# Kernel tuning notes

Hardware: AMD Instinct MI355X
Metric: run time of the kernel (lower is better)

The kernel has to match this reference:

```python
import jax, jax.numpy as jnp
import numpy as np

DIM = 128
K = 16


def knn_points(xyz, new_xyz, k):
    # squared-distance matrix [B, M, N]
    dist = -2.0 * jnp.einsum('bmd,bnd->bmn', new_xyz, xyz)
    dist = dist + jnp.sum(new_xyz ** 2, -1, keepdims=True)
    dist = dist + jnp.sum(xyz ** 2, -1)[:, None, :]
    _, idx = jax.lax.top_k(-dist, k)  # smallest distances
    return idx  # [B, M, k]


def index_points(points, idx):
    # points [B, N, C], idx [B, M, k] -> [B, M, k, C]
    B, M, k = idx.shape
    C = points.shape[-1]
    flat = jnp.take_along_axis(points, idx.reshape(B, M * k, 1), axis=1)
    return flat.reshape(B, M, k, C)


def linear(x, w, b):
    return x @ w + b


def setup_inputs() -> dict:
    key = jax.random.key(0)
    ks = jax.random.split(key, 16)
    s = 0.02
    d = DIM
    inp = {
        'xyz': jax.random.normal(ks[0], (2, 8192, 3), jnp.float32),
        'features': jax.random.normal(ks[1], (2, 8192, d), jnp.float32),
        'wq': jax.random.normal(ks[2], (d, d), jnp.float32) * s,
        'bq': jnp.zeros((d,), jnp.float32),
        'wk': jax.random.normal(ks[3], (d, d), jnp.float32) * s,
        'bk': jnp.zeros((d,), jnp.float32),
        'wv': jax.random.normal(ks[4], (d, d), jnp.float32) * s,
        'bv': jnp.zeros((d,), jnp.float32),
        'pos_w1': jax.random.normal(ks[5], (3, d), jnp.float32) * s,
        'pos_b1': jnp.zeros((d,), jnp.float32),
        'pos_w2': jax.random.normal(ks[6], (d, d), jnp.float32) * s,
        'pos_b2': jnp.zeros((d,), jnp.float32),
        'attn_w1': jax.random.normal(ks[7], (d, d), jnp.float32) * s,
        'attn_b1': jnp.zeros((d,), jnp.float32),
        'attn_w2': jax.random.normal(ks[8], (d, d), jnp.float32) * s,
        'attn_b2': jnp.zeros((d,), jnp.float32),
    }
    return inp


def reference(xyz, features, wq, bq, wk, bk, wv, bv,
              pos_w1, pos_b1, pos_w2, pos_b2,
              attn_w1, attn_b1, attn_w2, attn_b2):
    idx = knn_points(xyz, xyz, K)  # [B, N, K]
    q = linear(features, wq, bq)
    k = linear(features, wk, bk)
    v = linear(features, wv, bv)
    k_g = index_points(k, idx)      # [B, N, K, C]
    v_g = index_points(v, idx)      # [B, N, K, C]
    xyz_g = index_points(xyz, idx)  # [B, N, K, 3]
    pos_diff = xyz[:, :, None, :] - xyz_g
    delta = linear(jax.nn.relu(linear(pos_diff, pos_w1, pos_b1)), pos_w2, pos_b2)
    attn_in = q[:, :, None, :] - k_g + delta
    attn = linear(jax.nn.relu(linear(attn_in, attn_w1, attn_b1)), attn_w2, attn_b2)
    attn = jax.nn.softmax(attn, axis=2)  # softmax over neighbor axis, per channel
    out = jnp.sum(attn * (v_g + delta), axis=2)  # [B, N, C]
    return out
```

## Files before the change

kernel.cpp:

```cpp
#include <hip/hip_runtime.h>
#include <math.h>

typedef unsigned short u16;
typedef unsigned int u32;
typedef __attribute__((ext_vector_type(8))) short short8b;
typedef __attribute__((ext_vector_type(4))) float f32x4;

#define N_PTS 8192
#define NTOT 16384
#define D 128
#define KNN 16
#define NCH_M 8
#define NCH_S 16
#define CAP 20

__device__ __forceinline__ u16 f2bf(float x) {
    u32 u = __float_as_uint(x);
    u = (u + 0x7FFFu + ((u >> 16) & 1u)) >> 16;
    return (u16)u;
}
__device__ __forceinline__ float bf2f(u16 v) {
    return __uint_as_float(((u32)v) << 16);
}

__global__ __launch_bounds__(256) void xyz4_prep(const float* __restrict__ xyz,
                                                 float4* __restrict__ xyz4) {
    const int i = blockIdx.x * 256 + threadIdx.x;
    const float x = xyz[i * 3 + 0], y = xyz[i * 3 + 1], z = xyz[i * 3 + 2];
    xyz4[i] = make_float4(x, y, z, 0.5f * (x * x + y * y + z * z));
}

__global__ __launch_bounds__(128) void knn_minslots(const float4* __restrict__ xyz4,
                                                    float* __restrict__ pmins) {
    __shared__ float4 tile[1024];
    const int tid = threadIdx.x;
    const int qA = blockIdx.x * 256 + tid;
    const int qB = qA + 128;
    const int cbase = (qA >> 13) * N_PTS + blockIdx.y * 1024;

    const float4 a = xyz4[qA];
    const float4 b = xyz4[qB];

    for (int i = tid; i < 1024; i += 128) tile[i] = xyz4[cbase + i];
    __syncthreads();

    float sA[16], sB[16];
#pragma unroll
    for (int s = 0; s < 16; ++s) { sA[s] = 1e30f; sB[s] = 1e30f; }

    for (int j0 = 0; j0 < 1024; j0 += 16) {
#pragma unroll
        for (int s = 0; s < 16; ++s) {
            const float4 c = tile[j0 + s];
            const float eA = fmaf(-a.x, c.x, fmaf(-a.y, c.y, fmaf(-a.z, c.z, c.w)));
            const float eB = fmaf(-b.x, c.x, fmaf(-b.y, c.y, fmaf(-b.z, c.z, c.w)));
            sA[s] = fminf(sA[s], eA);
            sB[s] = fminf(sB[s], eB);
        }
    }
#pragma unroll
    for (int s = 0; s < 16; ++s) {
        pmins[(size_t)(blockIdx.y * 16 + s) * NTOT + qA] = sA[s];
        pmins[(size_t)(blockIdx.y * 16 + s) * NTOT + qB] = sB[s];
    }
}

__global__ __launch_bounds__(256) void knn_thresh(const float* __restrict__ pmins,
                                                  float* __restrict__ thr) {
    const int g = blockIdx.x * 256 + threadIdx.x;
    float m[16];
#pragma unroll
    for (int s = 0; s < 16; ++s) m[s] = 1e30f;
    for (int ch = 0; ch < NCH_M; ++ch) {
#pragma unroll
        for (int s = 0; s < 16; ++s)
            m[s] = fminf(m[s], pmins[(size_t)(ch * 16 + s) * NTOT + g]);
    }
    float T = m[0];
#pragma unroll
    for (int s = 1; s < 16; ++s) T = fmaxf(T, m[s]);
    u32 u = __float_as_uint(T);
    u = (T >= 0.f) ? (u + 1u) : (u - 1u);
    thr[g] = __uint_as_float(u);
}

__global__ __launch_bounds__(256) void knn_select(const float4* __restrict__ xyz4,
                                                  const float* __restrict__ thr,
                                                  float* __restrict__ dcomp,
                                                  u16* __restrict__ jcomp) {
    __shared__ float4 tile[512];
    const int tid = threadIdx.x;
    const int ch = blockIdx.y;
    const int qA = blockIdx.x * 512 + tid;
    const int qB = qA + 256;
    const int cbase = (qA >> 13) * N_PTS + ch * 512;

    const float4 a = xyz4[qA];
    const float4 b = xyz4[qB];
    const float tA = thr[qA];
    const float tB = thr[qB];

    for (int i = tid; i < 512; i += 256) tile[i] = xyz4[cbase + i];
    __syncthreads();

    int cntA = 0, cntB = 0;
#pragma unroll 8
    for (int j = 0; j < 512; ++j) {
        const float4 c = tile[j];
        const float eA = fmaf(-a.x, c.x, fmaf(-a.y, c.y, fmaf(-a.z, c.z, c.w)));
        const float eB = fmaf(-b.x, c.x, fmaf(-b.y, c.y, fmaf(-b.z, c.z, c.w)));
        if (eA < tA) {
            if (cntA < CAP) {
                dcomp[(size_t)(ch * CAP + cntA) * NTOT + qA] = eA;
                jcomp[(size_t)(ch * CAP + cntA) * NTOT + qA] = (u16)j;
            }
            ++cntA;
        }
        if (eB < tB) {
            if (cntB < CAP) {
                dcomp[(size_t)(ch * CAP + cntB) * NTOT + qB] = eB;
                jcomp[(size_t)(ch * CAP + cntB) * NTOT + qB] = (u16)j;
            }
            ++cntB;
        }
    }
    for (int t = min(cntA, CAP); t < CAP; ++t)
        dcomp[(size_t)(ch * CAP + t) * NTOT + qA] = 1e30f;
    for (int t = min(cntB, CAP); t < CAP; ++t)
        dcomp[(size_t)(ch * CAP + t) * NTOT + qB] = 1e30f;
}

__global__ __launch_bounds__(64) void knn_merge(const float* __restrict__ dcomp,
                                                const u16* __restrict__ jcomp,
                                                int* __restrict__ knn_out) {
    const int g = blockIdx.x * 64 + threadIdx.x;
    const int bbase = (g >> 13) * N_PTS;
    float dist[KNN];
    int idx[KNN];
#pragma unroll
    for (int s = 0; s < KNN; ++s) { dist[s] = 1e30f; idx[s] = 0; }

    for (int ch = 0; ch < NCH_S; ++ch) {
        float d[CAP];
        int jj[CAP];
#pragma unroll
        for (int t = 0; t < CAP; ++t) {
            d[t] = dcomp[(size_t)(ch * CAP + t) * NTOT + g];
            jj[t] = (int)jcomp[(size_t)(ch * CAP + t) * NTOT + g];
        }
#pragma unroll
        for (int t = 0; t < CAP; ++t) {
            if (d[t] < dist[KNN - 1]) {
                dist[KNN - 1] = d[t];
                idx[KNN - 1] = bbase + ch * 512 + jj[t];
#pragma unroll
                for (int s = KNN - 1; s > 0; --s) {
                    if (dist[s] < dist[s - 1]) {
                        const float td = dist[s]; dist[s] = dist[s - 1]; dist[s - 1] = td;
                        const int ti = idx[s]; idx[s] = idx[s - 1]; idx[s - 1] = ti;
                    }
                }
            }
        }
    }
#pragma unroll
    for (int s = 0; s < KNN; ++s) knn_out[g * KNN + s] = idx[s];
}

__global__ __launch_bounds__(256) void qkv_kernel(const float* __restrict__ feat,
                                                  const float* __restrict__ wq, const float* __restrict__ bq,
                                                  const float* __restrict__ wk, const float* __restrict__ bk,
                                                  const float* __restrict__ wv, const float* __restrict__ bv,
                                                  float* __restrict__ qbuf, u16* __restrict__ kb,
                                                  u16* __restrict__ vb) {
    __shared__ float ftile[64][D];
    const int r0 = blockIdx.x * 64;

    const float* src = feat + (size_t)r0 * D;
    for (int i = threadIdx.x; i < 64 * D / 4; i += 256) {
        ((float4*)&ftile[0][0])[i] = ((const float4*)src)[i];
    }
    __syncthreads();

    const int col = threadIdx.x & (D - 1);
    const int rbase = (threadIdx.x >> 7) * 32;

    float accq[32], acck[32], accv[32];
    const float bqv = bq[col], bkv = bk[col], bvv = bv[col];
#pragma unroll
    for (int r = 0; r < 32; ++r) { accq[r] = bqv; acck[r] = bkv; accv[r] = bvv; }

    for (int i = 0; i < D; i += 4) {
        const float wq0 = wq[(i + 0) * D + col], wq1 = wq[(i + 1) * D + col];
        const float wq2 = wq[(i + 2) * D + col], wq3 = wq[(i + 3) * D + col];
        const float wk0 = wk[(i + 0) * D + col], wk1 = wk[(i + 1) * D + col];
        const float wk2 = wk[(i + 2) * D + col], wk3 = wk[(i + 3) * D + col];
        const float wv0 = wv[(i + 0) * D + col], wv1 = wv[(i + 1) * D + col];
        const float wv2 = wv[(i + 2) * D + col], wv3 = wv[(i + 3) * D + col];
#pragma unroll
        for (int r = 0; r < 32; ++r) {
            const float4 f = *(const float4*)&ftile[rbase + r][i];
            accq[r] = fmaf(f.x, wq0, accq[r]); accq[r] = fmaf(f.y, wq1, accq[r]);
            accq[r] = fmaf(f.z, wq2, accq[r]); accq[r] = fmaf(f.w, wq3, accq[r]);
            acck[r] = fmaf(f.x, wk0, acck[r]); acck[r] = fmaf(f.y, wk1, acck[r]);
            acck[r] = fmaf(f.z, wk2, acck[r]); acck[r] = fmaf(f.w, wk3, acck[r]);
            accv[r] = fmaf(f.x, wv0, accv[r]); accv[r] = fmaf(f.y, wv1, accv[r]);
            accv[r] = fmaf(f.z, wv2, accv[r]); accv[r] = fmaf(f.w, wv3, accv[r]);
        }
    }
#pragma unroll
    for (int r = 0; r < 32; ++r) {
        const size_t o = (size_t)(r0 + rbase + r) * D + col;
        qbuf[o] = accq[r]; kb[o] = f2bf(acck[r]); vb[o] = f2bf(accv[r]);
    }
}

__global__ __launch_bounds__(256) void pack_w(const float* __restrict__ pw2,
                                              const float* __restrict__ aw1,
                                              const float* __restrict__ aw2,
                                              u16* __restrict__ wp) {
    const int i = blockIdx.x * 256 + threadIdx.x;
    const int m = i >> 14;
    const int r = i & 16383;
    const int j = r & 7, l = (r >> 3) & 63, t = (r >> 9) & 7, q = r >> 12;
    const float* w = (m == 0) ? pw2 : (m == 1) ? aw1 : aw2;
    wp[i] = f2bf(w[(q * 32 + 8 * (l >> 4) + j) * D + t * 16 + (l & 15)]);
}

__device__ __forceinline__ void gemm_tile(const char* atile, const u16* wl, int mat,
                                          const float* brow, int a, int c2, int lane,
                                          f32x4 acc[2][2]) {
    const int c16 = lane & 15, grp = lane >> 4;
#pragma unroll
    for (int mt = 0; mt < 2; ++mt)
#pragma unroll
        for (int ct = 0; ct < 2; ++ct) {
            const float b = brow[c2 * 32 + ct * 16 + c16];
            acc[mt][ct] = (f32x4){b, b, b, b};
        }
#pragma unroll
    for (int q = 0; q < 4; ++q) {
        short8b af[2], bf[2];
#pragma unroll
        for (int mt = 0; mt < 2; ++mt) {
            const int row = (2 * a + mt) * 16 + c16;
            const int byte = (row * 256 + (q * 32 + grp * 8) * 2) ^ ((row & 7) << 4);
            af[mt] = *(const short8b*)(atile + byte);
        }
#pragma unroll
        for (int ct = 0; ct < 2; ++ct) {
            const int tg = c2 * 2 + ct;
            bf[ct] = *(const short8b*)((const char*)wl + (size_t)mat * 32768 +
                                       (size_t)((q * 8 + tg) * 64 + lane) * 16);
        }
#pragma unroll
        for (int mt = 0; mt < 2; ++mt)
#pragma unroll
            for (int ct = 0; ct < 2; ++ct)
                acc[mt][ct] = __builtin_amdgcn_mfma_f32_16x16x32_bf16(af[mt], bf[ct], acc[mt][ct], 0, 0, 0);
    }
}

__global__ __launch_bounds__(1024, 4) void fused_v3(const float* __restrict__ xyz,
                                                    const float* __restrict__ qbuf,
                                                    const u16* __restrict__ kb,
                                                    const u16* __restrict__ vb,
                                                    const int* __restrict__ knn_in,
                                                    const u16* __restrict__ wpack,
                                                    const float* __restrict__ pw1,
                                                    const float* __restrict__ pb1,
                                                    const float* __restrict__ pb2,
                                                    const float* __restrict__ ab1,
                                                    const float* __restrict__ ab2,
                                                    float* __restrict__ out) {
    __shared__ __align__(16) u16 wlds[49152];
    __shared__ __align__(16) char atile[32768];
    __shared__ float pw1s[3][D];
    __shared__ float pb1s[D];
    __shared__ float bias[3][D];
    __shared__ float diffs[128][4];
    __shared__ int nbrs[128];

    const int tid = threadIdx.x;
    {
        const uint4* s = (const uint4*)wpack;
        uint4* d = (uint4*)wlds;
        for (int i = tid; i < 6144; i += 1024) d[i] = s[i];
        if (tid < 384) pw1s[tid >> 7][tid & 127] = pw1[tid];
        if (tid < 128) pb1s[tid] = pb1[tid];
        else if (tid < 256) bias[0][tid & 127] = pb2[tid & 127];
        else if (tid < 512 && tid >= 384) bias[1][tid & 127] = ab1[tid & 127];
        else if (tid >= 512 && tid < 640) bias[2][tid & 127] = ab2[tid & 127];
    }

    const int wid = tid >> 6, lane = tid & 63;
    const int a = wid >> 2, c2 = wid & 3;
    const int c16 = lane & 15, grp = lane >> 4;

    for (int g = 0; g < 8; ++g) {
        const int p0 = blockIdx.x * 64 + g * 8;
        __syncthreads();

        if (tid < 128) {
            const int pt = p0 + (tid >> 4);
            const int nb = knn_in[pt * KNN + (tid & 15)];
            nbrs[tid] = nb;
            diffs[tid][0] = xyz[pt * 3 + 0] - xyz[nb * 3 + 0];
            diffs[tid][1] = xyz[pt * 3 + 1] - xyz[nb * 3 + 1];
            diffs[tid][2] = xyz[pt * 3 + 2] - xyz[nb * 3 + 2];
        }
        __syncthreads();

        {
            const int row = tid >> 3;
            const int c0 = (tid & 7) * 16;
            const float d0 = diffs[row][0], d1 = diffs[row][1], d2 = diffs[row][2];
#pragma unroll
            for (int c = 0; c < 16; c += 2) {
                const int cc = c0 + c;
                float h0 = pb1s[cc];
                h0 = fmaf(d0, pw1s[0][cc], h0); h0 = fmaf(d1, pw1s[1][cc], h0); h0 = fmaf(d2, pw1s[2][cc], h0);
                float h1 = pb1s[cc + 1];
                h1 = fmaf(d0, pw1s[0][cc + 1], h1); h1 = fmaf(d1, pw1s[1][cc + 1], h1); h1 = fmaf(d2, pw1s[2][cc + 1], h1);
                const u32 packed = (u32)f2bf(fmaxf(h0, 0.f)) | ((u32)f2bf(fmaxf(h1, 0.f)) << 16);
                const int byte = (row * 256 + cc * 2) ^ ((row & 7) << 4);
                *(u32*)(atile + byte) = packed;
            }
        }
        __syncthreads();

        f32x4 del[2][2];
        gemm_tile(atile, wlds, 0, bias[0], a, c2, lane, del);
        __syncthreads();

#pragma unroll
        for (int mt = 0; mt < 2; ++mt) {
            const int pt = p0 + 2 * a + mt;
#pragma unroll
            for (int ct = 0; ct < 2; ++ct) {
                const int col = c2 * 32 + ct * 16 + c16;
                const float qv = qbuf[(size_t)pt * D + col];
#pragma unroll
                for (int r = 0; r < 4; ++r) {
                    const int lrow = (2 * a + mt) * 16 + grp * 4 + r;
                    const int nb = nbrs[lrow];
                    const float kg = bf2f(kb[(size_t)nb * D + col]);
                    const float v = qv - kg + del[mt][ct][r];
                    const int byte = (lrow * 256 + col * 2) ^ ((lrow & 7) << 4);
                    *(u16*)(atile + byte) = f2bf(v);
                }
            }
        }
        __syncthreads();

        f32x4 acc[2][2];
        gemm_tile(atile, wlds, 1, bias[1], a, c2, lane, acc);
        __syncthreads();

#pragma unroll
        for (int mt = 0; mt < 2; ++mt)
#pragma unroll
            for (int ct = 0; ct < 2; ++ct) {
                const int col = c2 * 32 + ct * 16 + c16;
#pragma unroll
                for (int r = 0; r < 4; ++r) {
                    const int lrow = (2 * a + mt) * 16 + grp * 4 + r;
                    const int byte = (lrow * 256 + col * 2) ^ ((lrow & 7) << 4);
                    *(u16*)(atile + byte) = f2bf(fmaxf(acc[mt][ct][r], 0.f));
                }
            }
        __syncthreads();

        gemm_tile(atile, wlds, 2, bias[2], a, c2, lane, acc);

        float om[2][2];
#pragma unroll
        for (int mt = 0; mt < 2; ++mt) {
#pragma unroll
            for (int ct = 0; ct < 2; ++ct) {
                const int col = c2 * 32 + ct * 16 + c16;
                float vg[4];
#pragma unroll
                for (int r = 0; r < 4; ++r) {
                    const int lrow = (2 * a + mt) * 16 + grp * 4 + r;
                    vg[r] = bf2f(vb[(size_t)nbrs[lrow] * D + col]);
                }
                float m = fmaxf(fmaxf(acc[mt][ct][0], acc[mt][ct][1]),
                                fmaxf(acc[mt][ct][2], acc[mt][ct][3]));
                m = fmaxf(m, __shfl_xor(m, 16));
                m = fmaxf(m, __shfl_xor(m, 32));
                float e[4], s = 0.f;
#pragma unroll
                for (int r = 0; r < 4; ++r) { e[r] = __expf(acc[mt][ct][r] - m); s += e[r]; }
                s += __shfl_xor(s, 16);
                s += __shfl_xor(s, 32);
                const float inv = 1.f / s;
                float o = 0.f;
#pragma unroll
                for (int r = 0; r < 4; ++r) o = fmaf(e[r] * inv, vg[r] + del[mt][ct][r], o);
                o += __shfl_xor(o, 16);
                o += __shfl_xor(o, 32);
                om[mt][ct] = o;
            }
        }
        float osel = om[0][0];
        if (grp == 1) osel = om[0][1];
        if (grp == 2) osel = om[1][0];
        if (grp == 3) osel = om[1][1];
        const int opt = p0 + 2 * a + (grp >> 1);
        out[(size_t)opt * D + c2 * 32 + (grp & 1) * 16 + c16] = osel;
    }
}

extern "C" void kernel_launch(void* const* d_in, const int* in_sizes, int n_in,
                              void* d_out, int out_size, void* d_ws, size_t ws_size,
                              hipStream_t stream) {
    const float* xyz = (const float*)d_in[0];
    const float* feat = (const float*)d_in[1];
    const float* wq = (const float*)d_in[2];
    const float* bq = (const float*)d_in[3];
    const float* wk = (const float*)d_in[4];
    const float* bk = (const float*)d_in[5];
    const float* wv = (const float*)d_in[6];
    const float* bv = (const float*)d_in[7];
    const float* pw1 = (const float*)d_in[8];
    const float* pb1 = (const float*)d_in[9];
    const float* pw2 = (const float*)d_in[10];
    const float* pb2 = (const float*)d_in[11];
    const float* aw1 = (const float*)d_in[12];
    const float* ab1 = (const float*)d_in[13];
    const float* aw2 = (const float*)d_in[14];
    const float* ab2 = (const float*)d_in[15];

    float* ws = (float*)d_ws;
    float* dcomp = ws;
    float* pmins = ws;
    u16* jcomp = (u16*)(ws + 5242880);
    float* thr = ws + 8126464;
    int* knn = (int*)(ws + 8142848);
    float4* xyz4 = (float4*)(ws + 8404992);
    float* qbuf = ws;
    u16* kb = (u16*)(ws + 2097152);
    u16* vb = (u16*)(ws + 3145728);
    u16* wpack = (u16*)(ws + 4194304);
    float* out = (float*)d_out;

    hipLaunchKernelGGL(xyz4_prep, dim3(64), dim3(256), 0, stream, xyz, xyz4);
    hipLaunchKernelGGL(knn_minslots, dim3(64, NCH_M), dim3(128), 0, stream, xyz4, pmins);
    hipLaunchKernelGGL(knn_thresh, dim3(64), dim3(256), 0, stream, pmins, thr);
    hipLaunchKernelGGL(knn_select, dim3(32, NCH_S), dim3(256), 0, stream,
                       xyz4, thr, dcomp, jcomp);
    hipLaunchKernelGGL(knn_merge, dim3(256), dim3(64), 0, stream, dcomp, jcomp, knn);
    hipLaunchKernelGGL(qkv_kernel, dim3(256), dim3(256), 0, stream,
                       feat, wq, bq, wk, bk, wv, bv, qbuf, kb, vb);
    hipLaunchKernelGGL(pack_w, dim3(192), dim3(256), 0, stream, pw2, aw1, aw2, wpack);
    hipLaunchKernelGGL(fused_v3, dim3(256), dim3(1024), 0, stream,
                       xyz, qbuf, kb, vb, knn, wpack,
                       pw1, pb1, pb2, ab1, ab2, out);
}
```

Before: 316.1 us.

## Restructure kNN and fused attention kernels with register-held weights and wider tiles

The kNN min-slot and select kernels now handle four queries per thread, with more chunks in the min-slot stage, so each shared-memory candidate load is reused across more queries. The qkv GEMM halves rows per block to raise the block count. The fused attention kernel moves from 1024 to 512 threads per block. It keeps the three packed MFMA weight matrices in registers rather than LDS and gives each wave four M-tiles. It also writes bf16 pairs into LDS via lane shuffles as 32-bit stores. These changes aim to cut LDS traffic and redundant loads, but the much larger register footprint could lower occupancy or cause spills.

```diff
diff --git a/kernel.cpp b/kernel.cpp
--- a/kernel.cpp
+++ b/kernel.cpp
@@ -10,7 +10,7 @@
 #define NTOT 16384
 #define D 128
 #define KNN 16
-#define NCH_M 8
+#define NCH_M 16
 #define NCH_S 16
 #define CAP 20
 
@@ -30,38 +30,43 @@
     xyz4[i] = make_float4(x, y, z, 0.5f * (x * x + y * y + z * z));
 }
 
-__global__ __launch_bounds__(128) void knn_minslots(const float4* __restrict__ xyz4,
+__global__ __launch_bounds__(256) void knn_minslots(const float4* __restrict__ xyz4,
                                                     float* __restrict__ pmins) {
-    __shared__ float4 tile[1024];
+    __shared__ float4 tile[512];
     const int tid = threadIdx.x;
-    const int qA = blockIdx.x * 256 + tid;
-    const int qB = qA + 128;
-    const int cbase = (qA >> 13) * N_PTS + blockIdx.y * 1024;
+    const int qbase = blockIdx.x * 1024;
+    const int qA = qbase + tid, qB = qA + 256, qC = qA + 512, qD = qA + 768;
+    const int cbase = (qbase >> 13) * N_PTS + blockIdx.y * 512;
 
     const float4 a = xyz4[qA];
     const float4 b = xyz4[qB];
-
-    for (int i = tid; i < 1024; i += 128) tile[i] = xyz4[cbase + i];
+    const float4 c4 = xyz4[qC];
+    const float4 d4 = xyz4[qD];
+
+    for (int i = tid; i < 512; i += 256) tile[i] = xyz4[cbase + i];
     __syncthreads();
 
-    float sA[16], sB[16];
-#pragma unroll
-    for (int s = 0; s < 16; ++s) { sA[s] = 1e30f; sB[s] = 1e30f; }
-
-    for (int j0 = 0; j0 < 1024; j0 += 16) {
+    float sA[16], sB[16], sC[16], sD[16];
+#pragma unroll
+    for (int s = 0; s < 16; ++s) { sA[s] = 1e30f; sB[s] = 1e30f; sC[s] = 1e30f; sD[s] = 1e30f; }
+
+    for (int j0 = 0; j0 < 512; j0 += 16) {
 #pragma unroll
         for (int s = 0; s < 16; ++s) {
             const float4 c = tile[j0 + s];
-            const float eA = fmaf(-a.x, c.x, fmaf(-a.y, c.y, fmaf(-a.z, c.z, c.w)));
-            const float eB = fmaf(-b.x, c.x, fmaf(-b.y, c.y, fmaf(-b.z, c.z, c.w)));
-            sA[s] = fminf(sA[s], eA);
-            sB[s] = fminf(sB[s], eB);
+            sA[s] = fminf(sA[s], fmaf(-a.x, c.x, fmaf(-a.y, c.y, fmaf(-a.z, c.z, c.w))));
+            sB[s] = fminf(sB[s], fmaf(-b.x, c.x, fmaf(-b.y, c.y, fmaf(-b.z, c.z, c.w))));
+            sC[s] = fminf(sC[s], fmaf(-c4.x, c.x, fmaf(-c4.y, c.y, fmaf(-c4.z, c.z, c.w))));
+            sD[s] = fminf(sD[s], fmaf(-d4.x, c.x, fmaf(-d4.y, c.y, fmaf(-d4.z, c.z, c.w))));
         }
     }
 #pragma unroll
     for (int s = 0; s < 16; ++s) {
-        pmins[(size_t)(blockIdx.y * 16 + s) * NTOT + qA] = sA[s];
-        pmins[(size_t)(blockIdx.y * 16 + s) * NTOT + qB] = sB[s];
+        const size_t rb = (size_t)(blockIdx.y * 16 + s) * NTOT;
+        pmins[rb + qA] = sA[s];
+        pmins[rb + qB] = sB[s];
+        pmins[rb + qC] = sC[s];
+        pmins[rb + qD] = sD[s];
     }
 }
 
@@ -91,43 +96,36 @@
     __shared__ float4 tile[512];
     const int tid = threadIdx.x;
     const int ch = blockIdx.y;
-    const int qA = blockIdx.x * 512 + tid;
-    const int qB = qA + 256;
-    const int cbase = (qA >> 13) * N_PTS + ch * 512;
+    const int qbase = blockIdx.x * 1024;
+    const int qA = qbase + tid, qB = qA + 256, qC = qA + 512, qD = qA + 768;
+    const int cbase = (qbase >> 13) * N_PTS + ch * 512;
 
     const float4 a = xyz4[qA];
     const float4 b = xyz4[qB];
-    const float tA = thr[qA];
-    const float tB = thr[qB];
+    const float4 c4 = xyz4[qC];
+    const float4 d4 = xyz4[qD];
+    const float tA = thr[qA], tB = thr[qB], tC = thr[qC], tD = thr[qD];
 
     for (int i = tid; i < 512; i += 256) tile[i] = xyz4[cbase + i];
     __syncthreads();
 
-    int cntA = 0, cntB = 0;
-#pragma unroll 8
+    int cA = 0, cB = 0, cC = 0, cD = 0;
+#pragma unroll 4
     for (int j = 0; j < 512; ++j) {
         const float4 c = tile[j];
         const float eA = fmaf(-a.x, c.x, fmaf(-a.y, c.y, fmaf(-a.z, c.z, c.w)));
         const float eB = fmaf(-b.x, c.x, fmaf(-b.y, c.y, fmaf(-b.z, c.z, c.w)));
-        if (eA < tA) {
-            if (cntA < CAP) {
-                dcomp[(size_t)(ch * CAP + cntA) * NTOT + qA] = eA;
-                jcomp[(size_t)(ch * CAP + cntA) * NTOT + qA] = (u16)j;
-            }
-            ++cntA;
-        }
-        if (eB < tB) {
-            if (cntB < CAP) {
-                dcomp[(size_t)(ch * CAP + cntB) * NTOT + qB] = eB;
-                jcomp[(size_t)(ch * CAP + cntB) * NTOT + qB] = (u16)j;
-            }
-            ++cntB;
-        }
-    }
-    for (int t = min(cntA, CAP); t < CAP; ++t)
-        dcomp[(size_t)(ch * CAP + t) * NTOT + qA] = 1e30f;
-    for (int t = min(cntB, CAP); t < CAP; ++t)
-        dcomp[(size_t)(ch * CAP + t) * NTOT + qB] = 1e30f;
+        const float eC = fmaf(-c4.x, c.x, fmaf(-c4.y, c.y, fmaf(-c4.z, c.z, c.w)));
+        const float eD = fmaf(-d4.x, c.x, fmaf(-d4.y, c.y, fmaf(-d4.z, c.z, c.w)));
+        if (eA < tA) { if (cA < CAP) { dcomp[(size_t)(ch * CAP + cA) * NTOT + qA] = eA; jcomp[(size_t)(ch * CAP + cA) * NTOT + qA] = (u16)j; } ++cA; }
+        if (eB < tB) { if (cB < CAP) { dcomp[(size_t)(ch * CAP + cB) * NTOT + qB] = eB; jcomp[(size_t)(ch * CAP + cB) * NTOT + qB] = (u16)j; } ++cB; }
+        if (eC < tC) { if (cC < CAP) { dcomp[(size_t)(ch * CAP + cC) * NTOT + qC] = eC; jcomp[(size_t)(ch * CAP + cC) * NTOT + qC] = (u16)j; } ++cC; }
+        if (eD < tD) { if (cD < CAP) { dcomp[(size_t)(ch * CAP + cD) * NTOT + qD] = eD; jcomp[(size_t)(ch * CAP + cD) * NTOT + qD] = (u16)j; } ++cD; }
+    }
+    for (int t = min(cA, CAP); t < CAP; ++t) dcomp[(size_t)(ch * CAP + t) * NTOT + qA] = 1e30f;
+    for (int t = min(cB, CAP); t < CAP; ++t) dcomp[(size_t)(ch * CAP + t) * NTOT + qB] = 1e30f;
+    for (int t = min(cC, CAP); t < CAP; ++t) dcomp[(size_t)(ch * CAP + t) * NTOT + qC] = 1e30f;
+    for (int t = min(cD, CAP); t < CAP; ++t) dcomp[(size_t)(ch * CAP + t) * NTOT + qD] = 1e30f;
 }
 
 __global__ __launch_bounds__(64) void knn_merge(const float* __restrict__ dcomp,
@@ -173,22 +171,22 @@
                                                   const float* __restrict__ wv, const float* __restrict__ bv,
                                                   float* __restrict__ qbuf, u16* __restrict__ kb,
                                                   u16* __restrict__ vb) {
-    __shared__ float ftile[64][D];
-    const int r0 = blockIdx.x * 64;
+    __shared__ float ftile[32][D];
+    const int r0 = blockIdx.x * 32;
 
     const float* src = feat + (size_t)r0 * D;
-    for (int i = threadIdx.x; i < 64 * D / 4; i += 256) {
+    for (int i = threadIdx.x; i < 32 * D / 4; i += 256) {
         ((float4*)&ftile[0][0])[i] = ((const float4*)src)[i];
     }
     __syncthreads();
 
     const int col = threadIdx.x & (D - 1);
-    const int rbase = (threadIdx.x >> 7) * 32;
-
-    float accq[32], acck[32], accv[32];
+    const int rbase = (threadIdx.x >> 7) * 16;
+
+    float accq[16], acck[16], accv[16];
     const float bqv = bq[col], bkv = bk[col], bvv = bv[col];
 #pragma unroll
-    for (int r = 0; r < 32; ++r) { accq[r] = bqv; acck[r] = bkv; accv[r] = bvv; }
+    for (int r = 0; r < 16; ++r) { accq[r] = bqv; acck[r] = bkv; accv[r] = bvv; }
 
     for (int i = 0; i < D; i += 4) {
         const float wq0 = wq[(i + 0) * D + col], wq1 = wq[(i + 1) * D + col];
@@ -198,7 +196,7 @@
         const float wv0 = wv[(i + 0) * D + col], wv1 = wv[(i + 1) * D + col];
         const float wv2 = wv[(i + 2) * D + col], wv3 = wv[(i + 3) * D + col];
 #pragma unroll
-        for (int r = 0; r < 32; ++r) {
+        for (int r = 0; r < 16; ++r) {
             const float4 f = *(const float4*)&ftile[rbase + r][i];
             accq[r] = fmaf(f.x, wq0, accq[r]); accq[r] = fmaf(f.y, wq1, accq[r]);
             accq[r] = fmaf(f.z, wq2, accq[r]); accq[r] = fmaf(f.w, wq3, accq[r]);
@@ -209,7 +207,7 @@
         }
     }
 #pragma unroll
-    for (int r = 0; r < 32; ++r) {
+    for (int r = 0; r < 16; ++r) {
         const size_t o = (size_t)(r0 + rbase + r) * D + col;
         qbuf[o] = accq[r]; kb[o] = f2bf(acck[r]); vb[o] = f2bf(accv[r]);
     }
@@ -227,12 +225,12 @@
     wp[i] = f2bf(w[(q * 32 + 8 * (l >> 4) + j) * D + t * 16 + (l & 15)]);
 }
 
-__device__ __forceinline__ void gemm_tile(const char* atile, const u16* wl, int mat,
-                                          const float* brow, int a, int c2, int lane,
-                                          f32x4 acc[2][2]) {
+__device__ __forceinline__ void gemm_reg(const char* atile, const short8b (&wf)[4][2],
+                                         const float* brow, int R, int c2, int lane,
+                                         f32x4 (&acc)[4][2]) {
     const int c16 = lane & 15, grp = lane >> 4;
 #pragma unroll
-    for (int mt = 0; mt < 2; ++mt)
+    for (int mt = 0; mt < 4; ++mt)
 #pragma unroll
         for (int ct = 0; ct < 2; ++ct) {
             const float b = brow[c2 * 32 + ct * 16 + c16];
@@ -240,40 +238,50 @@
         }
 #pragma unroll
     for (int q = 0; q < 4; ++q) {
-        short8b af[2], bf[2];
-#pragma unroll
-        for (int mt = 0; mt < 2; ++mt) {
-            const int row = (2 * a + mt) * 16 + c16;
+        short8b af[4];
+#pragma unroll
+        for (int mt = 0; mt < 4; ++mt) {
+            const int row = R * 64 + mt * 16 + c16;
             const int byte = (row * 256 + (q * 32 + grp * 8) * 2) ^ ((row & 7) << 4);
             af[mt] = *(const short8b*)(atile + byte);
         }
 #pragma unroll
-        for (int ct = 0; ct < 2; ++ct) {
-            const int tg = c2 * 2 + ct;
-            bf[ct] = *(const short8b*)((const char*)wl + (size_t)mat * 32768 +
-                                       (size_t)((q * 8 + tg) * 64 + lane) * 16);
-        }
-#pragma unroll
-        for (int mt = 0; mt < 2; ++mt)
+        for (int mt = 0; mt < 4; ++mt)
 #pragma unroll
             for (int ct = 0; ct < 2; ++ct)
-                acc[mt][ct] = __builtin_amdgcn_mfma_f32_16x16x32_bf16(af[mt], bf[ct], acc[mt][ct], 0, 0, 0);
-    }
-}
-
-__global__ __launch_bounds__(1024, 4) void fused_v3(const float* __restrict__ xyz,
-                                                    const float* __restrict__ qbuf,
-                                                    const u16* __restrict__ kb,
-                                                    const u16* __restrict__ vb,
-                                                    const int* __restrict__ knn_in,
-                                                    const u16* __restrict__ wpack,
-                                                    const float* __restrict__ pw1,
-                                                    const float* __restrict__ pb1,
-                                                    const float* __restrict__ pb2,
-                                                    const float* __restrict__ ab1,
-                                                    const float* __restrict__ ab2,
-                                                    float* __restrict__ out) {
-    __shared__ __align__(16) u16 wlds[49152];
+                acc[mt][ct] = __builtin_amdgcn_mfma_f32_16x16x32_bf16(af[mt], wf[q][ct], acc[mt][ct], 0, 0, 0);
+    }
+}
+
+__device__ __forceinline__ void pair_store(char* atile, int rowbase, int col, bool odd,
+                                           float v0, float v1, float v2, float v3) {
+    const float p0 = __shfl_xor(v0, 1), p1 = __shfl_xor(v1, 1);
+    const float p2 = __shfl_xor(v2, 1), p3 = __shfl_xor(v3, 1);
+    const u32 w0 = odd ? ((u32)f2bf(p0) | ((u32)f2bf(v0) << 16)) : ((u32)f2bf(v0) | ((u32)f2bf(p0) << 16));
+    const u32 w1 = odd ? ((u32)f2bf(p1) | ((u32)f2bf(v1) << 16)) : ((u32)f2bf(v1) | ((u32)f2bf(p1) << 16));
+    const u32 w2 = odd ? ((u32)f2bf(p2) | ((u32)f2bf(v2) << 16)) : ((u32)f2bf(v2) | ((u32)f2bf(p2) << 16));
+    const u32 w3 = odd ? ((u32)f2bf(p3) | ((u32)f2bf(v3) << 16)) : ((u32)f2bf(v3) | ((u32)f2bf(p3) << 16));
+    const int cb = (col & ~1) * 2;
+    const int ra = rowbase + (odd ? 2 : 0);
+    const int rb = ra + 1;
+    const u32 wa = odd ? w2 : w0;
+    const u32 wb = odd ? w3 : w1;
+    *(u32*)(atile + ((ra * 256 + cb) ^ ((ra & 7) << 4))) = wa;
+    *(u32*)(atile + ((rb * 256 + cb) ^ ((rb & 7) << 4))) = wb;
+}
+
+__global__ __launch_bounds__(512, 2) void fused_v4(const float* __restrict__ xyz,
+                                                   const float* __restrict__ qbuf,
+                                                   const u16* __restrict__ kb,
+                                                   const u16* __restrict__ vb,
+                                                   const int* __restrict__ knn_in,
+                                                   const u16* __restrict__ wpack,
+                                                   const float* __restrict__ pw1,
+                                                   const float* __restrict__ pb1,
+                                                   const float* __restrict__ pb2,
+                                                   const float* __restrict__ ab1,
+                                                   const float* __restrict__ ab2,
+                                                   float* __restrict__ out) {
     __shared__ __align__(16) char atile[32768];
     __shared__ float pw1s[3][D];
     __shared__ float pb1s[D];
@@ -282,20 +290,27 @@
     __shared__ int nbrs[128];
 
     const int tid = threadIdx.x;
-    {
-        const uint4* s = (const uint4*)wpack;
-        uint4* d = (uint4*)wlds;
-        for (int i = tid; i < 6144; i += 1024) d[i] = s[i];
-        if (tid < 384) pw1s[tid >> 7][tid & 127] = pw1[tid];
-        if (tid < 128) pb1s[tid] = pb1[tid];
-        else if (tid < 256) bias[0][tid & 127] = pb2[tid & 127];
-        else if (tid < 512 && tid >= 384) bias[1][tid & 127] = ab1[tid & 127];
-        else if (tid >= 512 && tid < 640) bias[2][tid & 127] = ab2[tid & 127];
-    }
+    if (tid < 384) pw1s[tid >> 7][tid & 127] = pw1[tid];
+    if (tid < 128) pb1s[tid] = pb1[tid];
+    else if (tid < 256) bias[0][tid & 127] = pb2[tid & 127];
+    else if (tid < 384) bias[1][tid & 127] = ab1[tid & 127];
+    else bias[2][tid & 127] = ab2[tid & 127];
 
     const int wid = tid >> 6, lane = tid & 63;
-    const int a = wid >> 2, c2 = wid & 3;
+    const int R = wid >> 2, c2 = wid & 3;
     const int c16 = lane & 15, grp = lane >> 4;
+    const bool odd = (c16 & 1) != 0;
+
+    short8b wf[3][4][2];
+#pragma unroll
+    for (int m = 0; m < 3; ++m)
+#pragma unroll
+        for (int q = 0; q < 4; ++q)
+#pragma unroll
+            for (int ct = 0; ct < 2; ++ct)
+                wf[m][q][ct] = *(const short8b*)(wpack + (size_t)m * 16384 +
+                                                 (size_t)((q * 8 + c2 * 2 + ct) * 64 + lane) * 8);
+    __syncthreads();
 
     for (int g = 0; g < 8; ++g) {
         const int p0 = blockIdx.x * 64 + g * 8;
@@ -312,11 +327,11 @@
         __syncthreads();
 
         {
-            const int row = tid >> 3;
-            const int c0 = (tid & 7) * 16;
+            const int row = tid >> 2;
+            const int c0 = (tid & 3) * 32;
             const float d0 = diffs[row][0], d1 = diffs[row][1], d2 = diffs[row][2];
 #pragma unroll
-            for (int c = 0; c < 16; c += 2) {
+            for (int c = 0; c < 32; c += 2) {
                 const int cc = c0 + c;
                 float h0 = pb1s[cc];
                 h0 = fmaf(d0, pw1s[0][cc], h0); h0 = fmaf(d1, pw1s[1][cc], h0); h0 = fmaf(d2, pw1s[2][cc], h0);
@@ -329,62 +344,59 @@
         }
         __syncthreads();
 
-        f32x4 del[2][2];
-        gemm_tile(atile, wlds, 0, bias[0], a, c2, lane, del);
-        __syncthreads();
-
-#pragma unroll
-        for (int mt = 0; mt < 2; ++mt) {
-            const int pt = p0 + 2 * a + mt;
+        f32x4 del[4][2];
+        gemm_reg(atile, wf[0], bias[0], R, c2, lane, del);
+        __syncthreads();
+
+#pragma unroll
+        for (int mt = 0; mt < 4; ++mt) {
+            const int pt = p0 + R * 4 + mt;
+            const int rowbase = R * 64 + mt * 16 + grp * 4;
 #pragma unroll
             for (int ct = 0; ct < 2; ++ct) {
                 const int col = c2 * 32 + ct * 16 + c16;
                 const float qv = qbuf[(size_t)pt * D + col];
+                float v[4];
 #pragma unroll
                 for (int r = 0; r < 4; ++r) {
-                    const int lrow = (2 * a + mt) * 16 + grp * 4 + r;
-                    const int nb = nbrs[lrow];
-                    const float kg = bf2f(kb[(size_t)nb * D + col]);
-                    const float v = qv - kg + del[mt][ct][r];
-                    const int byte = (lrow * 256 + col * 2) ^ ((lrow & 7) << 4);
-                    *(u16*)(atile + byte) = f2bf(v);
+                    const float kg = bf2f(kb[(size_t)nbrs[rowbase + r] * D + col]);
+                    v[r] = qv - kg + del[mt][ct][r];
                 }
+                pair_store(atile, rowbase, col, odd, v[0], v[1], v[2], v[3]);
             }
         }
         __syncthreads();
 
-        f32x4 acc[2][2];
-        gemm_tile(atile, wlds, 1, bias[1], a, c2, lane, acc);
-        __syncthreads();
-
-#pragma unroll
-        for (int mt = 0; mt < 2; ++mt)
+        f32x4 acc[4][2];
+        gemm_reg(atile, wf[1], bias[1], R, c2, lane, acc);
+        __syncthreads();
+
+#pragma unroll
+        for (int mt = 0; mt < 4; ++mt) {
+            const int rowbase = R * 64 + mt * 16 + grp * 4;
 #pragma unroll
             for (int ct = 0; ct < 2; ++ct) {
                 const int col = c2 * 32 + ct * 16 + c16;
-#pragma unroll
-                for (int r = 0; r < 4; ++r) {
-                    const int lrow = (2 * a + mt) * 16 + grp * 4 + r;
-                    const int byte = (lrow * 256 + col * 2) ^ ((lrow & 7) << 4);
-                    *(u16*)(atile + byte) = f2bf(fmaxf(acc[mt][ct][r], 0.f));
-                }
+                pair_store(atile, rowbase, col, odd,
+                           fmaxf(acc[mt][ct][0], 0.f), fmaxf(acc[mt][ct][1], 0.f),
+                           fmaxf(acc[mt][ct][2], 0.f), fmaxf(acc[mt][ct][3], 0.f));
             }
-        __syncthreads();
-
-        gemm_tile(atile, wlds, 2, bias[2], a, c2, lane, acc);
-
-        float om[2][2];
-#pragma unroll
-        for (int mt = 0; mt < 2; ++mt) {
+        }
+        __syncthreads();
+
+        gemm_reg(atile, wf[2], bias[2], R, c2, lane, acc);
+
+#pragma unroll
+        for (int mt = 0; mt < 4; ++mt) {
+            const int pt = p0 + R * 4 + mt;
+            const int rowbase = R * 64 + mt * 16 + grp * 4;
 #pragma unroll
             for (int ct = 0; ct < 2; ++ct) {
                 const int col = c2 * 32 + ct * 16 + c16;
                 float vg[4];
 #pragma unroll
-                for (int r = 0; r < 4; ++r) {
-                    const int lrow = (2 * a + mt) * 16 + grp * 4 + r;
-                    vg[r] = bf2f(vb[(size_t)nbrs[lrow] * D + col]);
-                }
+                for (int r = 0; r < 4; ++r)
+                    vg[r] = bf2f(vb[(size_t)nbrs[rowbase + r] * D + col]);
                 float m = fmaxf(fmaxf(acc[mt][ct][0], acc[mt][ct][1]),
                                 fmaxf(acc[mt][ct][2], acc[mt][ct][3]));
                 m = fmaxf(m, __shfl_xor(m, 16));
@@ -400,15 +412,9 @@
                 for (int r = 0; r < 4; ++r) o = fmaf(e[r] * inv, vg[r] + del[mt][ct][r], o);
                 o += __shfl_xor(o, 16);
                 o += __shfl_xor(o, 32);
-                om[mt][ct] = o;
+                if (grp == mt) out[(size_t)pt * D + col] = o;
             }
         }
-        float osel = om[0][0];
-        if (grp == 1) osel = om[0][1];
-        if (grp == 2) osel = om[1][0];
-        if (grp == 3) osel = om[1][1];
-        const int opt = p0 + 2 * a + (grp >> 1);
-        out[(size_t)opt * D + c2 * 32 + (grp & 1) * 16 + c16] = osel;
     }
 }
 
@@ -446,15 +452,15 @@
     float* out = (float*)d_out;
 
     hipLaunchKernelGGL(xyz4_prep, dim3(64), dim3(256), 0, stream, xyz, xyz4);
-    hipLaunchKernelGGL(knn_minslots, dim3(64, NCH_M), dim3(128), 0, stream, xyz4, pmins);
+    hipLaunchKernelGGL(knn_minslots, dim3(16, NCH_M), dim3(256), 0, stream, xyz4, pmins);
     hipLaunchKernelGGL(knn_thresh, dim3(64), dim3(256), 0, stream, pmins, thr);
-    hipLaunchKernelGGL(knn_select, dim3(32, NCH_S), dim3(256), 0, stream,
+    hipLaunchKernelGGL(knn_select, dim3(16, NCH_S), dim3(256), 0, stream,
                        xyz4, thr, dcomp, jcomp);
     hipLaunchKernelGGL(knn_merge, dim3(256), dim3(64), 0, stream, dcomp, jcomp, knn);
-    hipLaunchKernelGGL(qkv_kernel, dim3(256), dim3(256), 0, stream,
+    hipLaunchKernelGGL(qkv_kernel, dim3(512), dim3(256), 0, stream,
                        feat, wq, bq, wk, bk, wv, bv, qbuf, kb, vb);
     hipLaunchKernelGGL(pack_w, dim3(192), dim3(256), 0, stream, pw2, aw1, aw2, wpack);
-    hipLaunchKernelGGL(fused_v3, dim3(256), dim3(1024), 0, stream,
+    hipLaunchKernelGGL(fused_v4, dim3(256), dim3(512), 0, stream,
                        xyz, qbuf, kb, vb, knn, wpack,
                        pw1, pb1, pb2, ab1, ab2, out);
 }
```

After: 355.9 us. 12.6% more time.
